# Kernel optimization log

Measured on AMD Instinct MI355X. Metric: run time of the kernel, lower is better.

Reference implementation:

```python
import jax, jax.numpy as jnp
import numpy as np

N_NODES = 100000  # total nodes (60k type-a + 40k type-b)
N_EDGES = 3200000


def spmm(rows, cols, vals, x):
    # y[r] = sum_e vals[e] * x[cols[e]] for edges with rows[e] == r  (COO SpMM)
    return jax.ops.segment_sum(vals[:, None] * x[cols], rows, num_segments=N_NODES)


def setup_inputs() -> dict:
    key = jax.random.key(0)
    ks = jax.random.split(key, 12)
    d_a, d_b, n_hid, n_out = 256, 128, 256, 64
    s = lambda d: (1.0 / np.sqrt(d)).astype(np.float32)
    return {
        "x_a": jax.random.normal(ks[0], (60000, d_a), dtype=jnp.float32),
        "x_b": jax.random.normal(ks[1], (40000, d_b), dtype=jnp.float32),
        "rows": jax.random.randint(ks[2], (N_EDGES,), 0, N_NODES, dtype=jnp.int32),
        "cols": jax.random.randint(ks[3], (N_EDGES,), 0, N_NODES, dtype=jnp.int32),
        "vals": jax.random.uniform(ks[4], (N_EDGES,), dtype=jnp.float32),
        "W1a": jax.random.normal(ks[5], (d_a, n_hid), dtype=jnp.float32) * s(d_a),
        "b1a": jnp.zeros((n_hid,), dtype=jnp.float32),
        "W1b": jax.random.normal(ks[6], (d_b, n_hid), dtype=jnp.float32) * s(d_b),
        "b1b": jnp.zeros((n_hid,), dtype=jnp.float32),
        "Wf": jax.random.normal(ks[7], (n_hid, n_hid), dtype=jnp.float32) * s(n_hid),
        "bf": jnp.zeros((n_hid,), dtype=jnp.float32),
        "W2": jax.random.normal(ks[8], (n_hid, n_out), dtype=jnp.float32) * s(n_hid),
        "b2": jnp.zeros((n_out,), dtype=jnp.float32),
    }


def reference(x_a, x_b, rows, cols, vals, W1a, b1a, W1b, b1b, Wf, bf, W2, b2):
    # per-type Linear + ReLU (dropout p=0 -> identity in eval/reference)
    h_a = jax.nn.relu(x_a @ W1a + b1a)  # [60000, n_hid]
    h_b = jax.nn.relu(x_b @ W1b + b1b)  # [40000, n_hid]
    x = jnp.concatenate([h_a, h_b], axis=0)  # [N_NODES, n_hid]
    # hop - 1 = 1 intermediate hop: Linear -> SpMM -> ReLU
    x = x @ Wf + bf
    x = spmm(rows, cols, vals, x)
    x = jax.nn.relu(x)
    # output projection then final SpMM aggregation
    x = x @ W2 + b2
    x = spmm(rows, cols, vals, x)  # [N_NODES, n_out]
    return x
```

## Files before the change

kernel.cpp:

```cpp
#include <hip/hip_runtime.h>

#define NN 100000
#define NE 3200000
#define NA 60000
#define NB 40000
#define NHID 256
#define NOUT 64

#define RPB 64
#define NBUCK 1563
#define PBLK 256
#define CHUNK 12500

typedef unsigned short u16;
typedef unsigned int u32;
typedef __attribute__((ext_vector_type(8))) short short8;
typedef __attribute__((ext_vector_type(4))) float f32x4;

__device__ __forceinline__ float bf2f(u16 u) {
  return __uint_as_float(((u32)u) << 16);
}
__device__ __forceinline__ u16 f2bf(float f) {
  u32 u = __float_as_uint(f);
  u32 r = (u + 0x7fffu + ((u >> 16) & 1u)) >> 16;
  return (u16)r;
}
__device__ __forceinline__ float i8f(u32 dw, int b) {
  return (float)((int)(dw << (24 - 8 * b)) >> 24);
}

__device__ __forceinline__ void gload_lds16(const void* gsrc, void* ldst) {
  __builtin_amdgcn_global_load_lds(
      (const __attribute__((address_space(1))) void*)gsrc,
      (__attribute__((address_space(3))) void*)ldst, 16, 0, 0);
}

template <int BN, int RELU_OUT, int QUANT>
__global__ __launch_bounds__(256) void gemm_mfma(
    const u16* __restrict__ A, const u16* __restrict__ Bt,
    const float* __restrict__ bias, void* __restrict__ Cout,
    float* __restrict__ scales, int M, int N, int K) {
  constexpr int BM = 128;
  constexpr int FI = (BN == 128) ? 4 : 2;
  constexpr int WROWS = FI * 16;
  __shared__ __align__(16) u16 As[BM * 32];
  __shared__ __align__(16) u16 Bs[BN * 32];

  const int tid = threadIdx.x;
  const int w = tid >> 6;
  const int lane = tid & 63;
  const int bm = blockIdx.x * BM;
  const int bn = blockIdx.y * BN;
  const int wr = (BN == 128) ? (w >> 1) : w;
  const int wc = (BN == 128) ? (w & 1) : 0;

  f32x4 acc[FI][4];
#pragma unroll
  for (int i = 0; i < FI; ++i)
#pragma unroll
    for (int j = 0; j < 4; ++j) acc[i][j] = (f32x4)0.f;

  for (int k0 = 0; k0 < K; k0 += 32) {
#pragma unroll
    for (int s = 0; s < 2; ++s) {
      const int inst = w * 2 + s;
      const int row = inst * 16 + (lane >> 2);
      int rg = bm + row;
      if (rg > M - 1) rg = M - 1;
      const int c = (lane & 3) ^ ((row >> 1) & 3);
      gload_lds16(A + (size_t)rg * K + k0 + c * 8, &As[inst * 512]);
    }
    if (BN == 128) {
#pragma unroll
      for (int s = 0; s < 2; ++s) {
        const int inst = w * 2 + s;
        const int row = inst * 16 + (lane >> 2);
        const int c = (lane & 3) ^ ((row >> 1) & 3);
        gload_lds16(Bt + (size_t)(bn + row) * K + k0 + c * 8,
                    &Bs[inst * 512]);
      }
    } else {
      const int inst = w;
      const int row = inst * 16 + (lane >> 2);
      const int c = (lane & 3) ^ ((row >> 1) & 3);
      gload_lds16(Bt + (size_t)(bn + row) * K + k0 + c * 8, &Bs[inst * 512]);
    }
    __syncthreads();

    const int kc = lane >> 4;
    short8 af[FI], bfr[4];
#pragma unroll
    for (int i = 0; i < FI; ++i) {
      const int row = wr * WROWS + i * 16 + (lane & 15);
      const int ch = kc ^ ((row >> 1) & 3);
      af[i] = *reinterpret_cast<const short8*>(&As[row * 32 + ch * 8]);
    }
#pragma unroll
    for (int j = 0; j < 4; ++j) {
      const int row = wc * 64 + j * 16 + (lane & 15);
      const int ch = kc ^ ((row >> 1) & 3);
      bfr[j] = *reinterpret_cast<const short8*>(&Bs[row * 32 + ch * 8]);
    }
#pragma unroll
    for (int i = 0; i < FI; ++i)
#pragma unroll
      for (int j = 0; j < 4; ++j)
        acc[i][j] = __builtin_amdgcn_mfma_f32_16x16x32_bf16(af[i], bfr[j],
                                                            acc[i][j], 0, 0, 0);
    __syncthreads();
  }

  if constexpr (QUANT == 1) {
    float bv[4];
#pragma unroll
    for (int j = 0; j < 4; ++j)
      bv[j] = bias[bn + wc * 64 + j * 16 + (lane & 15)];
    const int g = (bn >> 6) + wc;
    u32* zq = (u32*)Cout;
#pragma unroll
    for (int i = 0; i < FI; ++i) {
#pragma unroll
      for (int r = 0; r < 4; ++r) {
        float o[4];
#pragma unroll
        for (int j = 0; j < 4; ++j) o[j] = acc[i][j][r] + bv[j];
        float am = fmaxf(fmaxf(fabsf(o[0]), fabsf(o[1])),
                         fmaxf(fabsf(o[2]), fabsf(o[3])));
#pragma unroll
        for (int mk = 1; mk < 16; mk <<= 1) am = fmaxf(am, __shfl_xor(am, mk));
        const float sinv = am > 0.f ? 127.f / am : 0.f;
        const float scv = am > 0.f ? am / 127.f : 0.f;
        const int q0 = __float2int_rn(o[0] * sinv);
        const int q1 = __float2int_rn(o[1] * sinv);
        const int q2 = __float2int_rn(o[2] * sinv);
        const int q3 = __float2int_rn(o[3] * sinv);
        const u32 dw = (q0 & 0xff) | ((q1 & 0xff) << 8) | ((q2 & 0xff) << 16) |
                       ((q3 & 0xff) << 24);
        const int row = bm + wr * WROWS + i * 16 + (lane >> 4) * 4 + r;
        if (row < M) {
          zq[(size_t)row * 64 + g * 16 + (lane & 15)] = dw;
          if ((lane & 15) == 0) scales[(size_t)row * 4 + g] = scv;
        }
      }
    }
  } else if constexpr (QUANT == 2) {
    float bv[4];
#pragma unroll
    for (int j = 0; j < 4; ++j) bv[j] = bias[j * 16 + (lane & 15)];
    u32* zq = (u32*)Cout;
#pragma unroll
    for (int i = 0; i < FI; ++i) {
#pragma unroll
      for (int r = 0; r < 4; ++r) {
        float o[4];
#pragma unroll
        for (int j = 0; j < 4; ++j) o[j] = acc[i][j][r] + bv[j];
        float am = fmaxf(fmaxf(fabsf(o[0]), fabsf(o[1])),
                         fmaxf(fabsf(o[2]), fabsf(o[3])));
#pragma unroll
        for (int mk = 1; mk < 16; mk <<= 1) am = fmaxf(am, __shfl_xor(am, mk));
        const float sinv = am > 0.f ? 127.f / am : 0.f;
        const float scv = am > 0.f ? am / 127.f : 0.f;
        const int q0 = __float2int_rn(o[0] * sinv);
        const int q1 = __float2int_rn(o[1] * sinv);
        const int q2 = __float2int_rn(o[2] * sinv);
        const int q3 = __float2int_rn(o[3] * sinv);
        const u32 dw = (q0 & 0xff) | ((q1 & 0xff) << 8) | ((q2 & 0xff) << 16) |
                       ((q3 & 0xff) << 24);
        const int row = bm + wr * WROWS + i * 16 + (lane >> 4) * 4 + r;
        if (row < M) {
          zq[(size_t)row * 16 + (lane & 15)] = dw;
          if ((lane & 15) == 0) scales[row] = scv;
        }
      }
    }
  } else {
    u16* C = (u16*)Cout;
#pragma unroll
    for (int i = 0; i < FI; ++i) {
#pragma unroll
      for (int j = 0; j < 4; ++j) {
        const int col = bn + wc * 64 + j * 16 + (lane & 15);
        const float bv = bias[col];
#pragma unroll
        for (int r = 0; r < 4; ++r) {
          const int row = bm + wr * WROWS + i * 16 + (lane >> 4) * 4 + r;
          if (row < M) {
            float o = acc[i][j][r] + bv;
            if (RELU_OUT) o = fmaxf(o, 0.f);
            C[(size_t)row * N + col] = f2bf(o);
          }
        }
      }
    }
  }
}

__global__ __launch_bounds__(256) void cvt_bf16(const float4* __restrict__ in,
                                                ushort4* __restrict__ out,
                                                int n4) {
  const int i = blockIdx.x * 256 + threadIdx.x;
  if (i >= n4) return;
  const float4 v = in[i];
  ushort4 o;
  o.x = f2bf(v.x); o.y = f2bf(v.y); o.z = f2bf(v.z); o.w = f2bf(v.w);
  out[i] = o;
}

__global__ __launch_bounds__(256) void wt_all(
    const float* __restrict__ W1a, const float* __restrict__ W1b,
    const float* __restrict__ Wf, const float* __restrict__ W2,
    u16* __restrict__ W1at, u16* __restrict__ W1bt, u16* __restrict__ Wft,
    u16* __restrict__ W2t) {
  const int i = blockIdx.x * 256 + threadIdx.x;
  if (i < 65536) {
    const int n = i >> 8, k = i & 255;
    W1at[i] = f2bf(W1a[k * 256 + n]);
  } else if (i < 98304) {
    const int t = i - 65536;
    const int n = t >> 7, k = t & 127;
    W1bt[t] = f2bf(W1b[k * 256 + n]);
  } else if (i < 163840) {
    const int t = i - 98304;
    const int n = t >> 8, k = t & 255;
    Wft[t] = f2bf(Wf[k * 256 + n]);
  } else if (i < 180224) {
    const int t = i - 163840;
    const int n = t >> 8, p = t & 255;
    const int f = ((p >> 6) << 6) + ((p & 3) << 4) + ((p >> 2) & 15);
    W2t[t] = f2bf(W2[f * 64 + n]);
  }
}

__global__ __launch_bounds__(256) void p1_hist(const int* __restrict__ rows,
                                               int* __restrict__ cnt) {
  __shared__ int h[NBUCK];
  const int tid = threadIdx.x;
  for (int i = tid; i < NBUCK; i += 256) h[i] = 0;
  __syncthreads();
  const int s = blockIdx.x * CHUNK;
  const int e = s + CHUNK;
  for (int i = s + tid; i < e; i += 256) atomicAdd(&h[rows[i] >> 6], 1);
  __syncthreads();
  for (int i = tid; i < NBUCK; i += 256) cnt[i * PBLK + blockIdx.x] = h[i];
}

__global__ __launch_bounds__(256) void s1_scan_blocks(int* __restrict__ cnt,
                                                      int* __restrict__ btot) {
  __shared__ int lds[256];
  const int bu = blockIdx.x;
  const int t = threadIdx.x;
  const int v = cnt[bu * PBLK + t];
  lds[t] = v;
  __syncthreads();
#pragma unroll
  for (int off = 1; off < 256; off <<= 1) {
    const int x = (t >= off) ? lds[t - off] : 0;
    __syncthreads();
    lds[t] += x;
    __syncthreads();
  }
  cnt[bu * PBLK + t] = lds[t] - v;
  if (t == 255) btot[bu] = lds[255];
}

__global__ __launch_bounds__(1024) void s2_scan_buckets(
    const int* __restrict__ btot, int* __restrict__ bstart) {
  __shared__ int lds[1024];
  __shared__ int carry;
  const int t = threadIdx.x;
  if (t == 0) carry = 0;
  __syncthreads();
  for (int base = 0; base < NBUCK; base += 1024) {
    const int i = base + t;
    const int v = (i < NBUCK) ? btot[i] : 0;
    lds[t] = v;
    __syncthreads();
#pragma unroll
    for (int off = 1; off < 1024; off <<= 1) {
      const int x = (t >= off) ? lds[t - off] : 0;
      __syncthreads();
      lds[t] += x;
      __syncthreads();
    }
    const int excl = lds[t] - v;
    const int c = carry;
    if (i < NBUCK) bstart[i] = c + excl;
    __syncthreads();
    if (t == 0) carry = c + lds[1023];
    __syncthreads();
  }
  if (t == 0) bstart[NBUCK] = NE;
}

__global__ __launch_bounds__(256) void p3_scatter(
    const int* __restrict__ rows, const int* __restrict__ cols,
    const float* __restrict__ vals, const int* __restrict__ cnt,
    const int* __restrict__ bstart, int2* __restrict__ edges) {
  __shared__ int lcur[NBUCK];
  const int tid = threadIdx.x;
  const int blk = blockIdx.x;
  for (int bu = tid; bu < NBUCK; bu += 256)
    lcur[bu] = bstart[bu] + cnt[bu * PBLK + blk];
  __syncthreads();
  const int s = blk * CHUNK;
  const int e = s + CHUNK;
  for (int i = s + tid; i < e; i += 256) {
    const int r = rows[i];
    const int bu = r >> 6;
    const int lr = r & 63;
    const int pos = atomicAdd(&lcur[bu], 1);
    edges[pos] = make_int2(cols[i] | (lr << 17), __float_as_int(vals[i]));
  }
}

__global__ __launch_bounds__(256) void sort_bucket(
    const int* __restrict__ bstart, const int2* __restrict__ edges,
    int2* __restrict__ edges2, int* __restrict__ rptr) {
  __shared__ int hist[RPB];
  __shared__ int sc[RPB];
  __shared__ int cur[RPB];
  const int bu = blockIdx.x;
  const int t = threadIdx.x;
  const int s = bstart[bu], e = bstart[bu + 1];
  if (t < RPB) hist[t] = 0;
  __syncthreads();
  for (int i = s + t; i < e; i += 256)
    atomicAdd(&hist[(edges[i].x >> 17) & 63], 1);
  __syncthreads();
  const int hv = (t < RPB) ? hist[t] : 0;
  if (t < RPB) sc[t] = hv;
  __syncthreads();
#pragma unroll
  for (int off = 1; off < RPB; off <<= 1) {
    const int x = (t >= off && t < RPB) ? sc[t - off] : 0;
    __syncthreads();
    if (t < RPB) sc[t] += x;
    __syncthreads();
  }
  if (t < RPB) {
    const int base = s + sc[t] - hv;
    cur[t] = base;
    const int grow = bu * RPB + t;
    if (grow < NN) rptr[grow] = base;
  }
  if (bu == 0 && t == 0) rptr[NN] = NE;
  __syncthreads();
  for (int i = s + t; i < e; i += 256) {
    const int2 ed = edges[i];
    const int lr = (ed.x >> 17) & 63;
    const int pos = atomicAdd(&cur[lr], 1);
    edges2[pos] = make_int2(ed.x & 0x1FFFF, ed.y);
  }
}

__global__ __launch_bounds__(256) void spmm256_q8(
    const int* __restrict__ ptr, const int2* __restrict__ edges,
    const u32* __restrict__ Zq, const float* __restrict__ scales,
    u16* __restrict__ Yb) {
  const int wid = (int)((blockIdx.x * (size_t)256 + threadIdx.x) >> 6);
  const int lane = threadIdx.x & 63;
  if (wid >= NN) return;
  const int s = ptr[wid], e = ptr[wid + 1];
  const int gsel = lane >> 4;
  float a0 = 0.f, a1 = 0.f, a2 = 0.f, a3 = 0.f;
  int j = s;
  for (; j + 7 < e; j += 8) {
    int2 ed[8];
#pragma unroll
    for (int q = 0; q < 8; ++q) ed[q] = edges[j + q];
    u32 dw[8];
    float sc[8];
#pragma unroll
    for (int q = 0; q < 8; ++q) {
      dw[q] = Zq[(size_t)ed[q].x * 64 + lane];
      sc[q] = scales[(size_t)ed[q].x * 4 + gsel];
    }
#pragma unroll
    for (int q = 0; q < 8; ++q) {
      const float vs = __int_as_float(ed[q].y) * sc[q];
      a0 += vs * i8f(dw[q], 0);
      a1 += vs * i8f(dw[q], 1);
      a2 += vs * i8f(dw[q], 2);
      a3 += vs * i8f(dw[q], 3);
    }
  }
  for (; j < e; ++j) {
    const int2 e0 = edges[j];
    const u32 dw = Zq[(size_t)e0.x * 64 + lane];
    const float vs =
        __int_as_float(e0.y) * scales[(size_t)e0.x * 4 + gsel];
    a0 += vs * i8f(dw, 0);
    a1 += vs * i8f(dw, 1);
    a2 += vs * i8f(dw, 2);
    a3 += vs * i8f(dw, 3);
  }
  ushort4 o;
  o.x = f2bf(fmaxf(a0, 0.f));
  o.y = f2bf(fmaxf(a1, 0.f));
  o.z = f2bf(fmaxf(a2, 0.f));
  o.w = f2bf(fmaxf(a3, 0.f));
  reinterpret_cast<ushort4*>(Yb + (size_t)wid * 256)[lane] = o;
}

__global__ __launch_bounds__(256) void spmm64_q8(
    const int* __restrict__ ptr, const int2* __restrict__ edges,
    const u32* __restrict__ Z2q, const float* __restrict__ zsc2,
    float* __restrict__ Y) {
  const int wid = (int)((blockIdx.x * (size_t)256 + threadIdx.x) >> 6);
  const int lane = threadIdx.x & 63;
  if (wid >= NN) return;
  const int s = ptr[wid], e = ptr[wid + 1];
  const int dwi = lane & 15;
  const int byi = lane >> 4;
  float acc = 0.f;
  int j = s;
  for (; j + 7 < e; j += 8) {
    int2 ed[8];
#pragma unroll
    for (int q = 0; q < 8; ++q) ed[q] = edges[j + q];
    u32 dw[8];
    float sc[8];
#pragma unroll
    for (int q = 0; q < 8; ++q) {
      dw[q] = Z2q[(size_t)ed[q].x * 16 + dwi];
      sc[q] = zsc2[ed[q].x];
    }
#pragma unroll
    for (int q = 0; q < 8; ++q)
      acc += __int_as_float(ed[q].y) * sc[q] * i8f(dw[q], byi);
  }
  for (; j < e; ++j) {
    const int2 e0 = edges[j];
    const u32 dw = Z2q[(size_t)e0.x * 16 + dwi];
    acc += __int_as_float(e0.y) * zsc2[e0.x] * i8f(dw, byi);
  }
  Y[(size_t)wid * 64 + lane] = acc;
}

extern "C" void kernel_launch(void* const* d_in, const int* in_sizes, int n_in,
                              void* d_out, int out_size, void* d_ws,
                              size_t ws_size, hipStream_t stream) {
  const float* x_a  = (const float*)d_in[0];
  const float* x_b  = (const float*)d_in[1];
  const int*   rows = (const int*)d_in[2];
  const int*   cols = (const int*)d_in[3];
  const float* vals = (const float*)d_in[4];
  const float* W1a  = (const float*)d_in[5];
  const float* b1a  = (const float*)d_in[6];
  const float* W1b  = (const float*)d_in[7];
  const float* b1b  = (const float*)d_in[8];
  const float* Wf   = (const float*)d_in[9];
  const float* bf   = (const float*)d_in[10];
  const float* W2   = (const float*)d_in[11];
  const float* b2   = (const float*)d_in[12];
  float* out = (float*)d_out;

  char* p = (char*)d_ws;
  u16* h    = (u16*)p;  p += (size_t)NN * NHID * 2;
  u32* zq   = (u32*)p;  p += (size_t)NN * 64 * 4;
  float* zscale = (float*)p; p += (size_t)NN * 4 * 4;
  u32* z2q  = (u32*)p;  p += (size_t)NN * 16 * 4;
  float* zsc2 = (float*)p; p += (size_t)NN * 4;
  u16* xab  = (u16*)p;  p += (size_t)NA * 256 * 2;
  u16* xbb  = (u16*)p;  p += (size_t)NB * 128 * 2;
  u16* W1at = (u16*)p;  p += 256 * 256 * 2;
  u16* W1bt = (u16*)p;  p += 256 * 128 * 2;
  u16* Wft  = (u16*)p;  p += 256 * 256 * 2;
  u16* W2t  = (u16*)p;  p += 64 * 256 * 2;
  int2* edges = (int2*)p; p += (size_t)NE * 8;
  int* cnt    = (int*)p;  p += (size_t)NBUCK * PBLK * 4;
  int* btot   = (int*)p;  p += (size_t)((NBUCK + 3) & ~3) * 4;
  int* bstart = (int*)p;  p += (size_t)((NBUCK + 4) & ~3) * 4;
  int* rptr   = (int*)p;  p += (size_t)(NN + 4) * 4;
  u16* s1b = h;
  int2* edges2 = (int2*)xab;

  cvt_bf16<<<(NA * 256 / 4 + 255) / 256, 256, 0, stream>>>(
      (const float4*)x_a, (ushort4*)xab, NA * 256 / 4);
  cvt_bf16<<<(NB * 128 / 4 + 255) / 256, 256, 0, stream>>>(
      (const float4*)x_b, (ushort4*)xbb, NB * 128 / 4);
  wt_all<<<704, 256, 0, stream>>>(W1a, W1b, Wf, W2, W1at, W1bt, Wft, W2t);

  gemm_mfma<128, 1, 0><<<dim3((NA + 127) / 128, 2), 256, 0, stream>>>(
      xab, W1at, b1a, h, nullptr, NA, NHID, 256);
  gemm_mfma<128, 1, 0><<<dim3((NB + 127) / 128, 2), 256, 0, stream>>>(
      xbb, W1bt, b1b, h + (size_t)NA * NHID, nullptr, NB, NHID, 128);
  gemm_mfma<128, 0, 1><<<dim3((NN + 127) / 128, 2), 256, 0, stream>>>(
      h, Wft, bf, zq, zscale, NN, NHID, 256);

  p1_hist<<<PBLK, 256, 0, stream>>>(rows, cnt);
  s1_scan_blocks<<<NBUCK, 256, 0, stream>>>(cnt, btot);
  s2_scan_buckets<<<1, 1024, 0, stream>>>(btot, bstart);
  p3_scatter<<<PBLK, 256, 0, stream>>>(rows, cols, vals, cnt, bstart, edges);
  sort_bucket<<<NBUCK, 256, 0, stream>>>(bstart, edges, edges2, rptr);

  spmm256_q8<<<(NN * 64 + 255) / 256, 256, 0, stream>>>(rptr, edges2, zq,
                                                        zscale, s1b);
  gemm_mfma<64, 0, 2><<<dim3((NN + 127) / 128, 1), 256, 0, stream>>>(
      s1b, W2t, b2, z2q, zsc2, NN, NOUT, 256);
  spmm64_q8<<<(NN * 64 + 255) / 256, 256, 0, stream>>>(rptr, edges2, z2q,
                                                       zsc2, out);
}
```

Before: 509.6 us.

## Merge independent prep, GEMM and scan stages into fewer horizontally fused launches

Folds the two input conversions, the weight transposes and the row histogram into one prep kernel. The layer-1 GEMMs now share a launch with the per-bucket block scan, and the Wf GEMM shares one with the bucket scan. The goal is to cut launch overhead and tail idle time by overlapping independent work within a single grid. The cost is branchy kernels whose block roles differ, shared LDS sizing, and a single-block serial scan that now sits alongside the GEMM blocks.

```diff
diff --git a/kernel.cpp b/kernel.cpp
--- a/kernel.cpp
+++ b/kernel.cpp
@@ -12,6 +12,12 @@
 #define PBLK 256
 #define CHUNK 12500
 
+#define CVT_BLKS 20000
+#define WT_BLKS 704
+#define G1_BLKS 938
+#define G2_BLKS 626
+#define G3_BLKS 1564
+
 typedef unsigned short u16;
 typedef unsigned int u32;
 typedef __attribute__((ext_vector_type(8))) short short8;
@@ -36,21 +42,18 @@
 }
 
 template <int BN, int RELU_OUT, int QUANT>
-__global__ __launch_bounds__(256) void gemm_mfma(
-    const u16* __restrict__ A, const u16* __restrict__ Bt,
+__device__ __forceinline__ void gemm_body(
+    int bx, int by, const u16* __restrict__ A, const u16* __restrict__ Bt,
     const float* __restrict__ bias, void* __restrict__ Cout,
-    float* __restrict__ scales, int M, int N, int K) {
-  constexpr int BM = 128;
+    float* __restrict__ scales, int M, int N, int K, u16* As, u16* Bs) {
   constexpr int FI = (BN == 128) ? 4 : 2;
   constexpr int WROWS = FI * 16;
-  __shared__ __align__(16) u16 As[BM * 32];
-  __shared__ __align__(16) u16 Bs[BN * 32];
 
   const int tid = threadIdx.x;
   const int w = tid >> 6;
   const int lane = tid & 63;
-  const int bm = blockIdx.x * BM;
-  const int bn = blockIdx.y * BN;
+  const int bm = bx * 128;
+  const int bn = by * BN;
   const int wr = (BN == 128) ? (w >> 1) : w;
   const int wc = (BN == 128) ? (w & 1) : 0;
 
@@ -196,101 +199,144 @@
   }
 }
 
-__global__ __launch_bounds__(256) void cvt_bf16(const float4* __restrict__ in,
-                                                ushort4* __restrict__ out,
-                                                int n4) {
-  const int i = blockIdx.x * 256 + threadIdx.x;
-  if (i >= n4) return;
-  const float4 v = in[i];
-  ushort4 o;
-  o.x = f2bf(v.x); o.y = f2bf(v.y); o.z = f2bf(v.z); o.w = f2bf(v.w);
-  out[i] = o;
-}
-
-__global__ __launch_bounds__(256) void wt_all(
+template <int BN, int RELU_OUT, int QUANT>
+__global__ __launch_bounds__(256) void gemm_mfma(
+    const u16* __restrict__ A, const u16* __restrict__ Bt,
+    const float* __restrict__ bias, void* __restrict__ Cout,
+    float* __restrict__ scales, int M, int N, int K) {
+  __shared__ __align__(16) u16 As[128 * 32];
+  __shared__ __align__(16) u16 Bs[BN * 32];
+  gemm_body<BN, RELU_OUT, QUANT>(blockIdx.x, blockIdx.y, A, Bt, bias, Cout,
+                                 scales, M, N, K, As, Bs);
+}
+
+__global__ __launch_bounds__(256) void prep(
+    const float4* __restrict__ xa, ushort4* __restrict__ xab4,
+    const float4* __restrict__ xb, ushort4* __restrict__ xbb4,
     const float* __restrict__ W1a, const float* __restrict__ W1b,
     const float* __restrict__ Wf, const float* __restrict__ W2,
     u16* __restrict__ W1at, u16* __restrict__ W1bt, u16* __restrict__ Wft,
-    u16* __restrict__ W2t) {
-  const int i = blockIdx.x * 256 + threadIdx.x;
-  if (i < 65536) {
-    const int n = i >> 8, k = i & 255;
-    W1at[i] = f2bf(W1a[k * 256 + n]);
-  } else if (i < 98304) {
-    const int t = i - 65536;
-    const int n = t >> 7, k = t & 127;
-    W1bt[t] = f2bf(W1b[k * 256 + n]);
-  } else if (i < 163840) {
-    const int t = i - 98304;
-    const int n = t >> 8, k = t & 255;
-    Wft[t] = f2bf(Wf[k * 256 + n]);
-  } else if (i < 180224) {
-    const int t = i - 163840;
-    const int n = t >> 8, p = t & 255;
-    const int f = ((p >> 6) << 6) + ((p & 3) << 4) + ((p >> 2) & 15);
-    W2t[t] = f2bf(W2[f * 64 + n]);
-  }
-}
-
-__global__ __launch_bounds__(256) void p1_hist(const int* __restrict__ rows,
-                                               int* __restrict__ cnt) {
-  __shared__ int h[NBUCK];
+    u16* __restrict__ W2t, const int* __restrict__ rows,
+    int* __restrict__ cnt) {
+  __shared__ int hsh[NBUCK];
+  const int b = blockIdx.x;
   const int tid = threadIdx.x;
-  for (int i = tid; i < NBUCK; i += 256) h[i] = 0;
-  __syncthreads();
-  const int s = blockIdx.x * CHUNK;
-  const int e = s + CHUNK;
-  for (int i = s + tid; i < e; i += 256) atomicAdd(&h[rows[i] >> 6], 1);
-  __syncthreads();
-  for (int i = tid; i < NBUCK; i += 256) cnt[i * PBLK + blockIdx.x] = h[i];
-}
-
-__global__ __launch_bounds__(256) void s1_scan_blocks(int* __restrict__ cnt,
-                                                      int* __restrict__ btot) {
-  __shared__ int lds[256];
-  const int bu = blockIdx.x;
-  const int t = threadIdx.x;
-  const int v = cnt[bu * PBLK + t];
-  lds[t] = v;
-  __syncthreads();
-#pragma unroll
-  for (int off = 1; off < 256; off <<= 1) {
-    const int x = (t >= off) ? lds[t - off] : 0;
-    __syncthreads();
-    lds[t] += x;
-    __syncthreads();
-  }
-  cnt[bu * PBLK + t] = lds[t] - v;
-  if (t == 255) btot[bu] = lds[255];
-}
-
-__global__ __launch_bounds__(1024) void s2_scan_buckets(
-    const int* __restrict__ btot, int* __restrict__ bstart) {
-  __shared__ int lds[1024];
-  __shared__ int carry;
-  const int t = threadIdx.x;
-  if (t == 0) carry = 0;
-  __syncthreads();
-  for (int base = 0; base < NBUCK; base += 1024) {
-    const int i = base + t;
-    const int v = (i < NBUCK) ? btot[i] : 0;
+  if (b < CVT_BLKS) {
+    const int i = b * 256 + tid;
+    const int na4 = NA * 64;
+    if (i < na4) {
+      const float4 v = xa[i];
+      ushort4 o;
+      o.x = f2bf(v.x); o.y = f2bf(v.y); o.z = f2bf(v.z); o.w = f2bf(v.w);
+      xab4[i] = o;
+    } else {
+      const int t = i - na4;
+      const float4 v = xb[t];
+      ushort4 o;
+      o.x = f2bf(v.x); o.y = f2bf(v.y); o.z = f2bf(v.z); o.w = f2bf(v.w);
+      xbb4[t] = o;
+    }
+  } else if (b < CVT_BLKS + WT_BLKS) {
+    const int i = (b - CVT_BLKS) * 256 + tid;
+    if (i < 65536) {
+      const int n = i >> 8, k = i & 255;
+      W1at[i] = f2bf(W1a[k * 256 + n]);
+    } else if (i < 98304) {
+      const int t = i - 65536;
+      const int n = t >> 7, k = t & 127;
+      W1bt[t] = f2bf(W1b[k * 256 + n]);
+    } else if (i < 163840) {
+      const int t = i - 98304;
+      const int n = t >> 8, k = t & 255;
+      Wft[t] = f2bf(Wf[k * 256 + n]);
+    } else if (i < 180224) {
+      const int t = i - 163840;
+      const int n = t >> 8, p = t & 255;
+      const int f = ((p >> 6) << 6) + ((p & 3) << 4) + ((p >> 2) & 15);
+      W2t[t] = f2bf(W2[f * 64 + n]);
+    }
+  } else {
+    const int blk = b - (CVT_BLKS + WT_BLKS);
+    for (int i = tid; i < NBUCK; i += 256) hsh[i] = 0;
+    __syncthreads();
+    const int s = blk * CHUNK;
+    const int e = s + CHUNK;
+    for (int i = s + tid; i < e; i += 256) atomicAdd(&hsh[rows[i] >> 6], 1);
+    __syncthreads();
+    for (int i = tid; i < NBUCK; i += 256) cnt[i * PBLK + blk] = hsh[i];
+  }
+}
+
+__global__ __launch_bounds__(256) void gemm12_s1(
+    const u16* __restrict__ xab, const u16* __restrict__ W1at,
+    const float* __restrict__ b1a, const u16* __restrict__ xbb,
+    const u16* __restrict__ W1bt, const float* __restrict__ b1b,
+    u16* __restrict__ h, int* __restrict__ cnt, int* __restrict__ btot) {
+  __shared__ __align__(16) u16 As[128 * 32];
+  __shared__ __align__(16) u16 Bs[128 * 32];
+  const int b = blockIdx.x;
+  if (b < G1_BLKS) {
+    gemm_body<128, 1, 0>(b % 469, b / 469, xab, W1at, b1a, h, nullptr, NA,
+                         NHID, 256, As, Bs);
+  } else if (b < G1_BLKS + G2_BLKS) {
+    const int t = b - G1_BLKS;
+    gemm_body<128, 1, 0>(t % 313, t / 313, xbb, W1bt, b1b,
+                         h + (size_t)NA * NHID, nullptr, NB, NHID, 128, As,
+                         Bs);
+  } else {
+    int* lds = (int*)As;
+    const int bu = b - (G1_BLKS + G2_BLKS);
+    const int t = threadIdx.x;
+    const int v = cnt[bu * PBLK + t];
     lds[t] = v;
     __syncthreads();
 #pragma unroll
-    for (int off = 1; off < 1024; off <<= 1) {
+    for (int off = 1; off < 256; off <<= 1) {
       const int x = (t >= off) ? lds[t - off] : 0;
       __syncthreads();
       lds[t] += x;
       __syncthreads();
     }
-    const int excl = lds[t] - v;
-    const int c = carry;
-    if (i < NBUCK) bstart[i] = c + excl;
-    __syncthreads();
-    if (t == 0) carry = c + lds[1023];
-    __syncthreads();
-  }
-  if (t == 0) bstart[NBUCK] = NE;
+    cnt[bu * PBLK + t] = lds[t] - v;
+    if (t == 255) btot[bu] = lds[255];
+  }
+}
+
+__global__ __launch_bounds__(256) void gemm3_s2(
+    const u16* __restrict__ h, const u16* __restrict__ Wft,
+    const float* __restrict__ bfv, u32* __restrict__ zq,
+    float* __restrict__ zscale, const int* __restrict__ btot,
+    int* __restrict__ bstart) {
+  __shared__ __align__(16) u16 As[128 * 32];
+  __shared__ __align__(16) u16 Bs[128 * 32];
+  const int b = blockIdx.x;
+  if (b < G3_BLKS) {
+    gemm_body<128, 0, 1>(b % 782, b / 782, h, Wft, bfv, zq, zscale, NN, NHID,
+                         256, As, Bs);
+  } else {
+    int* lds = (int*)As;
+    const int t = threadIdx.x;
+    int carry = 0;
+    for (int base = 0; base < NBUCK; base += 256) {
+      const int i = base + t;
+      const int v = (i < NBUCK) ? btot[i] : 0;
+      lds[t] = v;
+      __syncthreads();
+#pragma unroll
+      for (int off = 1; off < 256; off <<= 1) {
+        const int x = (t >= off) ? lds[t - off] : 0;
+        __syncthreads();
+        lds[t] += x;
+        __syncthreads();
+      }
+      const int excl = lds[t] - v;
+      const int tot = lds[255];
+      if (i < NBUCK) bstart[i] = carry + excl;
+      __syncthreads();
+      carry += tot;
+    }
+    if (t == 0) bstart[NBUCK] = NE;
+  }
 }
 
 __global__ __launch_bounds__(256) void p3_scatter(
@@ -476,22 +522,16 @@
   u16* s1b = h;
   int2* edges2 = (int2*)xab;
 
-  cvt_bf16<<<(NA * 256 / 4 + 255) / 256, 256, 0, stream>>>(
-      (const float4*)x_a, (ushort4*)xab, NA * 256 / 4);
-  cvt_bf16<<<(NB * 128 / 4 + 255) / 256, 256, 0, stream>>>(
-      (const float4*)x_b, (ushort4*)xbb, NB * 128 / 4);
-  wt_all<<<704, 256, 0, stream>>>(W1a, W1b, Wf, W2, W1at, W1bt, Wft, W2t);
-
-  gemm_mfma<128, 1, 0><<<dim3((NA + 127) / 128, 2), 256, 0, stream>>>(
-      xab, W1at, b1a, h, nullptr, NA, NHID, 256);
-  gemm_mfma<128, 1, 0><<<dim3((NB + 127) / 128, 2), 256, 0, stream>>>(
-      xbb, W1bt, b1b, h + (size_t)NA * NHID, nullptr, NB, NHID, 128);
-  gemm_mfma<128, 0, 1><<<dim3((NN + 127) / 128, 2), 256, 0, stream>>>(
-      h, Wft, bf, zq, zscale, NN, NHID, 256);
-
-  p1_hist<<<PBLK, 256, 0, stream>>>(rows, cnt);
-  s1_scan_blocks<<<NBUCK, 256, 0, stream>>>(cnt, btot);
-  s2_scan_buckets<<<1, 1024, 0, stream>>>(btot, bstart);
+  prep<<<CVT_BLKS + WT_BLKS + PBLK, 256, 0, stream>>>(
+      (const float4*)x_a, (ushort4*)xab, (const float4*)x_b, (ushort4*)xbb,
+      W1a, W1b, Wf, W2, W1at, W1bt, Wft, W2t, rows, cnt);
+
+  gemm12_s1<<<G1_BLKS + G2_BLKS + NBUCK, 256, 0, stream>>>(
+      xab, W1at, b1a, xbb, W1bt, b1b, h, cnt, btot);
+
+  gemm3_s2<<<G3_BLKS + 1, 256, 0, stream>>>(h, Wft, bf, zq, zscale, btot,
+                                            bstart);
+
   p3_scatter<<<PBLK, 256, 0, stream>>>(rows, cols, vals, cnt, bstart, edges);
   sort_bucket<<<NBUCK, 256, 0, stream>>>(bstart, edges, edges2, rptr);
 
```

Result: faster. 491.9 us (-3.5%).
